# Performance work log

Measured on AMD Instinct MI355X. Metric: run time of the kernel, lower is better.

The kernel has to match this reference:

```python
import jax, jax.numpy as jnp
import numpy as np
from jax import lax


def setup_inputs() -> dict:
    key = jax.random.key(0)
    feature = jax.random.normal(key, (16, 64, 256, 256), dtype=jnp.float32)
    return {"feature": feature, "dist": 1}


def _avg_pool_up(feature):
    # avg_pool2d(k=3, stride=2, pad=1, count_include_pad=True): always divide by 9
    summed = lax.reduce_window(
        feature, 0.0, lax.add,
        window_dimensions=(1, 1, 3, 3),
        window_strides=(1, 1, 2, 2),
        padding=((0, 0), (0, 0), (1, 1), (1, 1)),
    )
    pooled = summed / 9.0  # [B, C, H/2, W/2]
    # nearest-neighbor upsample x2 back to [B, C, H, W]
    return jnp.repeat(jnp.repeat(pooled, 2, axis=2), 2, axis=3)


def reference(feature, dist):
    d = 2 * dist
    up = _avg_pool_up(feature)
    # order matches torch concat: top_left, top, top_right, left, right, bot_left, bot, bot_right
    shifts = [(d, d), (d, 0), (d, -d), (0, d), (0, -d), (-d, d), (-d, 0), (-d, -d)]
    diff = None
    for s in shifts:
        sq = jnp.sum((feature - jnp.roll(up, s, axis=(2, 3))) ** 2, axis=1, keepdims=True)
        diff = sq if diff is None else jnp.maximum(diff, sq)
    return diff  # [B, 1, H, W]
```

## Files before the change

### kernel.cpp

```cpp
#include <hip/hip_runtime.h>


#define QR 4
#define MAXPR (QR + 10)

__global__ __launch_bounds__(512) void fused_k(const float* __restrict__ f,
                                               float* __restrict__ out,
                                               const int* __restrict__ distp) {
    __shared__ __align__(16) float ps[MAXPR][128];
    const int dist = *distp;
    const int PR   = QR + 2 * dist;

    const int band = blockIdx.x & 31;
    const int b    = blockIdx.x >> 5;
    const int ty0  = band * QR;
    const int tid  = threadIdx.x;
    const int qr   = tid >> 7;
    const int tx   = tid & 127;
    const int ty   = ty0 + qr;

    for (int w = tid; w < MAXPR * 128; w += 512) ((float*)ps)[w] = 0.f;
    __syncthreads();

    const float* fb = f + (size_t)b * 64 * 65536;
    const int foff = (2 * ty) * 256 + 2 * tx;

    const int cxm = (tx - dist) & 127;
    const int cxp = (tx + dist) & 127;
    const int rm  = qr;
    const int rc  = qr + dist;
    const int rp  = qr + 2 * dist;

    float dot[4][8], sp2[8], sf2[4];
#pragma unroll
    for (int q = 0; q < 4; ++q) { sf2[q] = 0.f;
#pragma unroll
        for (int n = 0; n < 8; ++n) dot[q][n] = 0.f; }
#pragma unroll
    for (int n = 0; n < 8; ++n) sp2[n] = 0.f;

    for (int c = 0; c < 64; ++c) {
        const float* fc = fb + (size_t)c * 65536;

        for (int w = tid; w < PR * 64; w += 512) {
            int r = w >> 6;
            int j = w & 63;
            int pr = (ty0 - dist + r) & 127;
            float s0 = 0.f, s1 = 0.f;
            int y0 = 2 * pr - 1;
#pragma unroll
            for (int ky = 0; ky < 3; ++ky) {
                int y = y0 + ky;
                if ((unsigned)y < 256u) {
                    const float* row = fc + y * 256 + 4 * j;
                    float  e = (j > 0) ? row[-1] : 0.f;
                    float4 v = *(const float4*)row;
                    s0 += e   + v.x + v.y;
                    s1 += v.y + v.z + v.w;
                }
            }
            *(float2*)&ps[r][2 * j] =
                make_float2(s0 * (1.f / 9.f), s1 * (1.f / 9.f));
        }
        __syncthreads();

        const float* fp = fc + foff;
        float2 q0 = *(const float2*)(fp);
        float2 q1 = *(const float2*)(fp + 256);
        float fv[4] = { q0.x, q0.y, q1.x, q1.y };

        float p[8];
        p[0] = ps[rm][cxm]; p[1] = ps[rm][tx]; p[2] = ps[rm][cxp];
        p[3] = ps[rc][cxm];                    p[4] = ps[rc][cxp];
        p[5] = ps[rp][cxm]; p[6] = ps[rp][tx]; p[7] = ps[rp][cxp];

#pragma unroll
        for (int n = 0; n < 8; ++n) sp2[n] = fmaf(p[n], p[n], sp2[n]);
#pragma unroll
        for (int q = 0; q < 4; ++q) {
            float fq = fv[q];
            sf2[q] = fmaf(fq, fq, sf2[q]);
#pragma unroll
            for (int n = 0; n < 8; ++n) dot[q][n] = fmaf(fq, p[n], dot[q][n]);
        }
        __syncthreads();
    }

    float res[4];
#pragma unroll
    for (int q = 0; q < 4; ++q) {
        float m = -3.4e38f;
#pragma unroll
        for (int n = 0; n < 8; ++n)
            m = fmaxf(m, fmaf(-2.f, dot[q][n], sf2[q] + sp2[n]));
        res[q] = m;
    }
    float* op = out + (size_t)b * 65536 + foff;
    *(float2*)(op)       = make_float2(res[0], res[1]);
    *(float2*)(op + 256) = make_float2(res[2], res[3]);
}

extern "C" void kernel_launch(void* const* d_in, const int* in_sizes, int n_in,
                              void* d_out, int out_size, void* d_ws, size_t ws_size,
                              hipStream_t stream) {
    const float* feature = (const float*)d_in[0];
    const int*   distp   = (const int*)d_in[1];
    float* out = (float*)d_out;

    fused_k<<<512, 512, 0, stream>>>(feature, out, distp);
}
```

Measured before the change: 416.5 us.

## Prefetch next channel's pooling rows and features into registers

```diff
diff --git a/kernel.cpp b/kernel.cpp
--- a/kernel.cpp
+++ b/kernel.cpp
@@ -4,9 +4,9 @@
 #define QR 4
 #define MAXPR (QR + 10)
 
-__global__ __launch_bounds__(512) void fused_k(const float* __restrict__ f,
-                                               float* __restrict__ out,
-                                               const int* __restrict__ distp) {
+__global__ __launch_bounds__(512, 4) void fused_k(const float* __restrict__ f,
+                                                  float* __restrict__ out,
+                                                  const int* __restrict__ distp) {
     __shared__ __align__(16) float ps[MAXPR][128];
     const int dist = *distp;
     const int PR   = QR + 2 * dist;
@@ -31,6 +31,12 @@
     const int rc  = qr + dist;
     const int rp  = qr + 2 * dist;
 
+    const bool havew = tid < PR * 64;
+    const int  r   = tid >> 6;
+    const int  j   = tid & 63;
+    const int  prr = (ty0 - dist + r) & 127;
+    const int  y0  = 2 * prr - 1;
+
     float dot[4][8], sp2[8], sf2[4];
 #pragma unroll
     for (int q = 0; q < 4; ++q) { sf2[q] = 0.f;
@@ -39,36 +45,76 @@
 #pragma unroll
     for (int n = 0; n < 8; ++n) sp2[n] = 0.f;
 
+    float4 pv0, pv1, pv2; float pe0, pe1, pe2;
+    float2 fqa, fqb;
+    {
+        const float* fc = fb;
+        pv0 = pv1 = pv2 = make_float4(0.f, 0.f, 0.f, 0.f);
+        pe0 = pe1 = pe2 = 0.f;
+#pragma unroll
+        for (int ky = 0; ky < 3; ++ky) {
+            int y = y0 + ky;
+            if (havew && (unsigned)y < 256u) {
+                const float* row = fc + y * 256 + 4 * j;
+                float  e = (j > 0) ? row[-1] : 0.f;
+                float4 v = *(const float4*)row;
+                if (ky == 0) { pv0 = v; pe0 = e; }
+                else if (ky == 1) { pv1 = v; pe1 = e; }
+                else { pv2 = v; pe2 = e; }
+            }
+        }
+        fqa = *(const float2*)(fc + foff);
+        fqb = *(const float2*)(fc + foff + 256);
+    }
+
     for (int c = 0; c < 64; ++c) {
-        const float* fc = fb + (size_t)c * 65536;
+        const int cn = (c + 1 < 64) ? c + 1 : 63;
+        const float* fcn = fb + (size_t)cn * 65536;
+        float4 nv0, nv1, nv2; float ne0, ne1, ne2;
+        nv0 = nv1 = nv2 = make_float4(0.f, 0.f, 0.f, 0.f);
+        ne0 = ne1 = ne2 = 0.f;
+#pragma unroll
+        for (int ky = 0; ky < 3; ++ky) {
+            int y = y0 + ky;
+            if (havew && (unsigned)y < 256u) {
+                const float* row = fcn + y * 256 + 4 * j;
+                float  e = (j > 0) ? row[-1] : 0.f;
+                float4 v = *(const float4*)row;
+                if (ky == 0) { nv0 = v; ne0 = e; }
+                else if (ky == 1) { nv1 = v; ne1 = e; }
+                else { nv2 = v; ne2 = e; }
+            }
+        }
+        float2 nfa = *(const float2*)(fcn + foff);
+        float2 nfb = *(const float2*)(fcn + foff + 256);
 
-        for (int w = tid; w < PR * 64; w += 512) {
-            int r = w >> 6;
-            int j = w & 63;
-            int pr = (ty0 - dist + r) & 127;
-            float s0 = 0.f, s1 = 0.f;
-            int y0 = 2 * pr - 1;
+        float s0 = (pe0 + pv0.x + pv0.y) + (pe1 + pv1.x + pv1.y) + (pe2 + pv2.x + pv2.y);
+        float s1 = (pv0.y + pv0.z + pv0.w) + (pv1.y + pv1.z + pv1.w) + (pv2.y + pv2.z + pv2.w);
+
+        __syncthreads();
+        if (havew)
+            *(float2*)&ps[r][2 * j] = make_float2(s0 * (1.f / 9.f), s1 * (1.f / 9.f));
+        for (int w = tid + 512; w < PR * 64; w += 512) {
+            int rr = w >> 6, jj = w & 63;
+            int pr2 = (ty0 - dist + rr) & 127;
+            float t0 = 0.f, t1 = 0.f;
+            int yy0 = 2 * pr2 - 1;
 #pragma unroll
             for (int ky = 0; ky < 3; ++ky) {
-                int y = y0 + ky;
+                int y = yy0 + ky;
                 if ((unsigned)y < 256u) {
-                    const float* row = fc + y * 256 + 4 * j;
-                    float  e = (j > 0) ? row[-1] : 0.f;
+                    const float* row = fb + (size_t)c * 65536 + y * 256 + 4 * jj;
+                    float  e = (jj > 0) ? row[-1] : 0.f;
                     float4 v = *(const float4*)row;
-                    s0 += e   + v.x + v.y;
-                    s1 += v.y + v.z + v.w;
+                    t0 += e   + v.x + v.y;
+                    t1 += v.y + v.z + v.w;
                 }
             }
-            *(float2*)&ps[r][2 * j] =
-                make_float2(s0 * (1.f / 9.f), s1 * (1.f / 9.f));
+            *(float2*)&ps[rr][2 * jj] = make_float2(t0 * (1.f / 9.f), t1 * (1.f / 9.f));
         }
         __syncthreads();
 
-        const float* fp = fc + foff;
-        float2 q0 = *(const float2*)(fp);
-        float2 q1 = *(const float2*)(fp + 256);
-        float fv[4] = { q0.x, q0.y, q1.x, q1.y };
-
+        float fv[4] = { fqa.x, fqa.y, fqb.x, fqb.y };
         float p[8];
         p[0] = ps[rm][cxm]; p[1] = ps[rm][tx]; p[2] = ps[rm][cxp];
         p[3] = ps[rc][cxm];                    p[4] = ps[rc][cxp];
@@ -83,7 +129,10 @@
 #pragma unroll
             for (int n = 0; n < 8; ++n) dot[q][n] = fmaf(fq, p[n], dot[q][n]);
         }
-        __syncthreads();
+
+        pv0 = nv0; pv1 = nv1; pv2 = nv2;
+        pe0 = ne0; pe1 = ne1; pe2 = ne2;
+        fqa = nfa; fqb = nfb;
     }
 
     float res[4];
```

Measured after the change: 377.8 us. 9.3% less time.

## Batch 16 channels per pooled-tile stage with a dist=1 specialized kernel

Applied to the files above, without the earlier changes.

```diff
diff --git a/kernel.cpp b/kernel.cpp
--- a/kernel.cpp
+++ b/kernel.cpp
@@ -1,15 +1,15 @@
 #include <hip/hip_runtime.h>
 
 
-#define QR 4
-#define MAXPR (QR + 10)
-
-__global__ __launch_bounds__(512) void fused_k(const float* __restrict__ f,
-                                               float* __restrict__ out,
-                                               const int* __restrict__ distp) {
-    __shared__ __align__(16) float ps[MAXPR][128];
-    const int dist = *distp;
-    const int PR   = QR + 2 * dist;
+#define NCH 16
+#define PR1 6
+#define QR  4
+
+__global__ __launch_bounds__(512, 4) void fused1_k(const float* __restrict__ f,
+                                                   float* __restrict__ out,
+                                                   const int* __restrict__ distp) {
+    if (*distp != 1) return;
+    __shared__ __align__(16) float ps[NCH][PR1][128];
 
     const int band = blockIdx.x & 31;
     const int b    = blockIdx.x >> 5;
@@ -19,17 +19,10 @@
     const int tx   = tid & 127;
     const int ty   = ty0 + qr;
 
-    for (int w = tid; w < MAXPR * 128; w += 512) ((float*)ps)[w] = 0.f;
-    __syncthreads();
-
     const float* fb = f + (size_t)b * 64 * 65536;
     const int foff = (2 * ty) * 256 + 2 * tx;
-
-    const int cxm = (tx - dist) & 127;
-    const int cxp = (tx + dist) & 127;
-    const int rm  = qr;
-    const int rc  = qr + dist;
-    const int rp  = qr + 2 * dist;
+    const int cxm = (tx - 1) & 127;
+    const int cxp = (tx + 1) & 127;
 
     float dot[4][8], sp2[8], sf2[4];
 #pragma unroll
@@ -39,15 +32,20 @@
 #pragma unroll
     for (int n = 0; n < 8; ++n) sp2[n] = 0.f;
 
-    for (int c = 0; c < 64; ++c) {
-        const float* fc = fb + (size_t)c * 65536;
-
-        for (int w = tid; w < PR * 64; w += 512) {
-            int r = w >> 6;
-            int j = w & 63;
-            int pr = (ty0 - dist + r) & 127;
+    for (int chunk = 0; chunk < 4; ++chunk) {
+        const float* fcb = fb + (size_t)chunk * NCH * 65536;
+
+#pragma unroll 4
+        for (int k = 0; k < 12; ++k) {
+            int idx = k * 512 + tid;
+            int ch  = idx / 384;
+            int rem = idx - ch * 384;
+            int r   = rem >> 6;
+            int j   = rem & 63;
+            int pr  = (ty0 - 1 + r) & 127;
+            const float* fc = fcb + (size_t)ch * 65536;
+            int y0 = 2 * pr - 1;
             float s0 = 0.f, s1 = 0.f;
-            int y0 = 2 * pr - 1;
 #pragma unroll
             for (int ky = 0; ky < 3; ++ky) {
                 int y = y0 + ky;
@@ -59,8 +57,111 @@
                     s1 += v.y + v.z + v.w;
                 }
             }
-            *(float2*)&ps[r][2 * j] =
+            *(float2*)&ps[ch][r][2 * j] =
                 make_float2(s0 * (1.f / 9.f), s1 * (1.f / 9.f));
+        }
+        __syncthreads();
+
+        float2 fa = *(const float2*)(fcb + foff);
+        float2 fbq = *(const float2*)(fcb + foff + 256);
+#pragma unroll 4
+        for (int ch = 0; ch < NCH; ++ch) {
+            float2 na = fa, nb = fbq;
+            if (ch + 1 < NCH) {
+                const float* fqn = fcb + (size_t)(ch + 1) * 65536 + foff;
+                na = *(const float2*)(fqn);
+                nb = *(const float2*)(fqn + 256);
+            }
+            float p[8];
+            p[0] = ps[ch][qr    ][cxm]; p[1] = ps[ch][qr    ][tx]; p[2] = ps[ch][qr    ][cxp];
+            p[3] = ps[ch][qr + 1][cxm];                            p[4] = ps[ch][qr + 1][cxp];
+            p[5] = ps[ch][qr + 2][cxm]; p[6] = ps[ch][qr + 2][tx]; p[7] = ps[ch][qr + 2][cxp];
+
+            float fv[4] = { fa.x, fa.y, fbq.x, fbq.y };
+#pragma unroll
+            for (int n = 0; n < 8; ++n) sp2[n] = fmaf(p[n], p[n], sp2[n]);
+#pragma unroll
+            for (int q = 0; q < 4; ++q) {
+                float fq = fv[q];
+                sf2[q] = fmaf(fq, fq, sf2[q]);
+#pragma unroll
+                for (int n = 0; n < 8; ++n) dot[q][n] = fmaf(fq, p[n], dot[q][n]);
+            }
+            fa = na; fbq = nb;
+        }
+        __syncthreads();
+    }
+
+    float res[4];
+#pragma unroll
+    for (int q = 0; q < 4; ++q) {
+        float m = -3.4e38f;
+#pragma unroll
+        for (int n = 0; n < 8; ++n)
+            m = fmaxf(m, fmaf(-2.f, dot[q][n], sf2[q] + sp2[n]));
+        res[q] = m;
+    }
+    float* op = out + (size_t)b * 65536 + foff;
+    *(float2*)(op)       = make_float2(res[0], res[1]);
+    *(float2*)(op + 256) = make_float2(res[2], res[3]);
+}
+
+#define MAXPR (QR + 10)
+
+__global__ __launch_bounds__(512, 4) void fusedg_k(const float* __restrict__ f,
+                                                   float* __restrict__ out,
+                                                   const int* __restrict__ distp) {
+    const int dist = *distp;
+    if (dist == 1) return;
+    __shared__ __align__(16) float ps[MAXPR][128];
+    const int PR   = QR + 2 * dist;
+
+    const int band = blockIdx.x & 31;
+    const int b    = blockIdx.x >> 5;
+    const int ty0  = band * QR;
+    const int tid  = threadIdx.x;
+    const int qr   = tid >> 7;
+    const int tx   = tid & 127;
+    const int ty   = ty0 + qr;
+
+    for (int w = tid; w < MAXPR * 128; w += 512) ((float*)ps)[w] = 0.f;
+    __syncthreads();
+
+    const float* fb = f + (size_t)b * 64 * 65536;
+    const int foff = (2 * ty) * 256 + 2 * tx;
+    const int cxm = (tx - dist) & 127;
+    const int cxp = (tx + dist) & 127;
+    const int rm  = qr;
+    const int rc  = qr + dist;
+    const int rp  = qr + 2 * dist;
+
+    float dot[4][8], sp2[8], sf2[4];
+#pragma unroll
+    for (int q = 0; q < 4; ++q) { sf2[q] = 0.f;
+#pragma unroll
+        for (int n = 0; n < 8; ++n) dot[q][n] = 0.f; }
+#pragma unroll
+    for (int n = 0; n < 8; ++n) sp2[n] = 0.f;
+
+    for (int c = 0; c < 64; ++c) {
+        const float* fc = fb + (size_t)c * 65536;
+        for (int w = tid; w < PR * 64; w += 512) {
+            int r = w >> 6, j = w & 63;
+            int pr = (ty0 - dist + r) & 127;
+            float s0 = 0.f, s1 = 0.f;
+            int y0 = 2 * pr - 1;
+#pragma unroll
+            for (int ky = 0; ky < 3; ++ky) {
+                int y = y0 + ky;
+                if ((unsigned)y < 256u) {
+                    const float* row = fc + y * 256 + 4 * j;
+                    float  e = (j > 0) ? row[-1] : 0.f;
+                    float4 v = *(const float4*)row;
+                    s0 += e   + v.x + v.y;
+                    s1 += v.y + v.z + v.w;
+                }
+            }
+            *(float2*)&ps[r][2 * j] = make_float2(s0 * (1.f / 9.f), s1 * (1.f / 9.f));
         }
         __syncthreads();
 
@@ -68,7 +169,6 @@
         float2 q0 = *(const float2*)(fp);
         float2 q1 = *(const float2*)(fp + 256);
         float fv[4] = { q0.x, q0.y, q1.x, q1.y };
-
         float p[8];
         p[0] = ps[rm][cxm]; p[1] = ps[rm][tx]; p[2] = ps[rm][cxp];
         p[3] = ps[rc][cxm];                    p[4] = ps[rc][cxp];
@@ -107,5 +207,6 @@
     const int*   distp   = (const int*)d_in[1];
     float* out = (float*)d_out;
 
-    fused_k<<<512, 512, 0, stream>>>(feature, out, distp);
+    fused1_k<<<512, 512, 0, stream>>>(feature, out, distp);
+    fusedg_k<<<512, 512, 0, stream>>>(feature, out, distp);
 }
```

New measurement: 393.5 us. -5.5%, faster.
